# Kernel tuning notes

Measured on AMD Instinct MI355X. Metric: run time of the kernel, lower is better.

Reference implementation:

```python
import jax, jax.numpy as jnp
import numpy as np
from functools import partial

B, C, H, W = 256, 3, 128, 128

def _conv(x, w, b, pad):
    y = jax.lax.conv_general_dilated(x, w, (1, 1), [(pad, pad), (pad, pad)],
                                     dimension_numbers=('NCHW', 'OIHW', 'NCHW'))
    return y + b[None, :, None, None]

def _maxpool2(x):
    return jax.lax.reduce_window(x, -jnp.inf, jax.lax.max, (1, 1, 2, 2), (1, 1, 2, 2), 'VALID')

def _linear(x, w, b):
    return x @ w.T + b

def _handcrafted(images):
    # uint8 quantization: floor(x*255); inputs in [0,1) so no wraparound
    img8 = jnp.floor(images * 255.0)                      # [B,3,H,W]
    brightness = img8.mean(axis=(-2, -1))                 # [B,3]
    contrast = img8.std(axis=(-2, -1))                    # [B,3] (ddof=0, numpy default)
    # cv2.Sobel ksize=3, BORDER_REFLECT_101 == jnp.pad 'reflect'; cv2 does correlation
    kx = jnp.array([[-1., 0., 1.], [-2., 0., 2.], [-1., 0., 1.]], dtype=img8.dtype)
    ky = kx.T
    k = jnp.stack([kx, ky])[:, None]                      # [2,1,3,3]
    p = jnp.pad(img8, ((0, 0), (0, 0), (1, 1), (1, 1)), mode='reflect')
    s = jax.lax.conv_general_dilated(p.reshape(B * 3, 1, H + 2, W + 2), k, (1, 1),
                                     'VALID', dimension_numbers=('NCHW', 'OIHW', 'NCHW'))
    edge = jnp.sqrt(s[:, 0] ** 2 + s[:, 1] ** 2).mean(axis=(-2, -1)).reshape(B, 3)
    return jnp.concatenate([edge, brightness, contrast], axis=1)  # [B,9]

def setup_inputs() -> dict:
    key = jax.random.key(0)
    ks = jax.random.split(key, 20)
    g = lambda i, shape, fan: (jax.random.normal(ks[i], shape, jnp.float32) * (1.0 / np.sqrt(fan)))
    return {
        'images': jax.random.uniform(ks[0], (B, C, H, W), jnp.float32),
        'W1': g(1, (32, 3, 3, 3), 27), 'b1': jnp.zeros((32,), jnp.float32),
        'W2': g(2, (64, 32, 3, 3), 288), 'b2': jnp.zeros((64,), jnp.float32),
        'Wa': g(3, (1, 64, 7, 7), 64 * 49), 'ba': jnp.zeros((1,), jnp.float32),
        'Wfc': g(4, (50, 64 * 32 * 32), 64 * 32 * 32), 'bfc': jnp.zeros((50,), jnp.float32),
        'Wh1': g(5, (32, 9), 9), 'bh1': jnp.zeros((32,), jnp.float32),
        'Wh2': g(6, (64, 32), 32), 'bh2': jnp.zeros((64,), jnp.float32),
        'Wh3': g(7, (50, 64), 64), 'bh3': jnp.zeros((50,), jnp.float32),
        'Wf': g(8, (64, 100), 100), 'bf': jnp.zeros((64,), jnp.float32),
        'Wc': g(9, (1, 64), 64), 'bc': jnp.zeros((1,), jnp.float32),
    }

def reference(images, W1, b1, W2, b2, Wa, ba, Wfc, bfc,
              Wh1, bh1, Wh2, bh2, Wh3, bh3, Wf, bf, Wc, bc):
    # CNN branch
    x = jax.nn.relu(_conv(images, W1, b1, 1))
    x = _maxpool2(x)
    x = jax.nn.relu(_conv(x, W2, b2, 1))
    x = _maxpool2(x)                                      # [B,64,32,32]
    attn = jax.nn.sigmoid(_conv(x, Wa, ba, 3))            # spatial attention
    x = x * attn
    cnn_feat = jax.nn.relu(_linear(x.reshape(B, -1), Wfc, bfc))  # [B,50]
    # handcrafted branch
    f = _handcrafted(images)                              # [B,9]
    h = jax.nn.relu(_linear(f, Wh1, bh1))
    h = jax.nn.relu(_linear(h, Wh2, bh2))
    h = jax.nn.relu(_linear(h, Wh3, bh3))                 # [B,50]
    fused = jax.nn.relu(_linear(jnp.concatenate([cnn_feat, h], axis=1), Wf, bf))
    logits = _linear(fused, Wc, bc)
    return jax.nn.sigmoid(logits)
```

## Files before the change

### kernel.cpp

```cpp
#include <hip/hip_runtime.h>
#include <stdint.h>

typedef __bf16 bf16x8 __attribute__((ext_vector_type(8)));
typedef float f32x4 __attribute__((ext_vector_type(4)));

__device__ inline float bf2f(uint16_t u) {
    uint32_t x = ((uint32_t)u) << 16;
    float f;
    __builtin_memcpy(&f, &x, 4);
    return f;
}
__device__ inline uint16_t f2bf(float f) {
    uint32_t x;
    __builtin_memcpy(&x, &f, 4);
    uint32_t r = (x + 0x7FFFu + ((x >> 16) & 1u)) >> 16;
    return (uint16_t)r;
}

__global__ __launch_bounds__(256) void k_prep_small(const float* __restrict__ W2,
                                                    const float* __restrict__ W1,
                                                    const float* __restrict__ Wa,
                                                    uint16_t* __restrict__ wA,
                                                    uint16_t* __restrict__ wA1c,
                                                    uint16_t* __restrict__ waP) {
    int bid = blockIdx.x;
    int tid = threadIdx.x;
    if (bid < 72) {
        int j = bid * 256 + tid;
        if (j >= 18432) return;
        int t = j >> 11, rem = j & 2047, oc = rem >> 5, ic = rem & 31;
        int dy = t / 3, dx = t - dy * 3;
        wA[j] = f2bf(W2[(oc * 32 + ic) * 9 + dy * 3 + dx]);
    } else if (bid < 84) {
        int j = (bid - 72) * 256 + tid;
        if (j >= 3072) return;
        int dy = j >> 10, rem = j & 1023, oc = rem >> 5, k = rem & 31;
        int dx = k >> 2, ic = k & 3;
        uint16_t v = 0;
        if (dx < 3 && ic < 3) v = f2bf(W1[((oc * 3 + ic) * 3 + dy) * 3 + dx]);
        wA1c[j] = v;
    } else {
        int j = (bid - 84) * 256 + tid;
        if (j >= 4096) return;
        int chunk = j >> 10, ks = (j >> 9) & 1, tl = (j >> 5) & 15, ch = j & 31;
        int t = chunk * 16 + tl;
        int cg = ks * 32 + ch;
        waP[j] = (t < 49) ? f2bf(Wa[cg * 49 + t]) : (uint16_t)0;
    }
}

__global__ __launch_bounds__(256) void k_prep_wfc(const float* __restrict__ Wfc,
                                                  uint16_t* __restrict__ wfcb) {
    __shared__ uint16_t sT[64][132];
    int o = blockIdx.x;
    int px0 = blockIdx.y * 128;
    int tid = threadIdx.x;
#pragma unroll
    for (int p = 0; p < 8; ++p) {
        int idx = p * 256 + tid;
        int ch = idx >> 5, c4 = idx & 31;
        float4 v = *(const float4*)&Wfc[(size_t)o * 65536 + ch * 1024 + px0 + c4 * 4];
        ushort4 u;
        u.x = f2bf(v.x);
        u.y = f2bf(v.y);
        u.z = f2bf(v.z);
        u.w = f2bf(v.w);
        *(ushort4*)&sT[ch][c4 * 4] = u;
    }
    __syncthreads();
#pragma unroll
    for (int p = 0; p < 8; ++p) {
        int idx = p * 256 + tid;
        int pxl = idx >> 4, c = idx & 15;
        ushort4 u;
        u.x = sT[4 * c + 0][pxl];
        u.y = sT[4 * c + 1][pxl];
        u.z = sT[4 * c + 2][pxl];
        u.w = sT[4 * c + 3][pxl];
        *(ushort4*)&wfcb[(size_t)o * 65536 + (size_t)(px0 + pxl) * 64 + c * 4] = u;
    }
}

__global__ __launch_bounds__(256) void k_handcrafted(const float* __restrict__ img,
                                                     float* __restrict__ f) {
    __shared__ float p[128 * 129];
    int c = blockIdx.x, b = blockIdx.y;
    const float* src = img + (((size_t)(b * 3 + c)) << 14);
    int tid = threadIdx.x;
    float sum = 0.f, sumsq = 0.f;
    for (int it = 0; it < 64; ++it) {
        int idx = tid + (it << 8);
        int r = idx >> 7, cc = idx & 127;
        float v = floorf(src[idx] * 255.0f);
        p[r * 129 + cc] = v;
        sum += v;
        sumsq += v * v;
    }
    __syncthreads();
    {
        int r = tid >> 1;
        int c0 = (tid & 1) * 64;
        int rm = (r == 0) ? 1 : (r - 1), rp = (r == 127) ? 126 : (r + 1);
        const float* Pm = &p[rm * 129];
        const float* P0 = &p[r * 129];
        const float* Pp = &p[rp * 129];
        float am, a0, ap, bm, b0, bp, cm, c0v, cp;
        if (c0 == 0) {
            a0 = Pm[0]; ap = Pm[1]; am = ap;
            b0 = P0[0]; bp = P0[1]; bm = bp;
            c0v = Pp[0]; cp = Pp[1]; cm = cp;
        } else {
            am = Pm[63]; a0 = Pm[64]; ap = Pm[65];
            bm = P0[63]; b0 = P0[64]; bp = P0[65];
            cm = Pp[63]; c0v = Pp[64]; cp = Pp[65];
        }
        float esum = 0.f;
        for (int i = 0; i < 64; ++i) {
            float gx = (ap - am) + 2.f * (bp - bm) + (cp - cm);
            float gy = (cm + 2.f * c0v + cp) - (am + 2.f * a0 + ap);
            esum += sqrtf(gx * gx + gy * gy);
            if (i < 63) {
                int nc = c0 + i + 2;
                am = a0; a0 = ap;
                bm = b0; b0 = bp;
                cm = c0v; c0v = cp;
                if (nc <= 127) {
                    ap = Pm[nc];
                    bp = P0[nc];
                    cp = Pp[nc];
                } else {
                    ap = am;
                    bp = bm;
                    cp = cm;
                }
            }
        }
        for (int off = 32; off; off >>= 1) {
            sum += __shfl_down(sum, off);
            sumsq += __shfl_down(sumsq, off);
            esum += __shfl_down(esum, off);
        }
        __syncthreads();
        int w = tid >> 6;
        if ((tid & 63) == 0) {
            p[w * 3 + 0] = sum;
            p[w * 3 + 1] = sumsq;
            p[w * 3 + 2] = esum;
        }
        __syncthreads();
        if (tid == 0) {
            float S = 0.f, Q = 0.f, E = 0.f;
            for (int i = 0; i < 4; ++i) {
                S += p[i * 3 + 0];
                Q += p[i * 3 + 1];
                E += p[i * 3 + 2];
            }
            const float inv = 1.0f / 16384.0f;
            float mean = S * inv;
            float var = Q * inv - mean * mean;
            f[b * 16 + c] = E * inv;
            f[b * 16 + 3 + c] = mean;
            f[b * 16 + 6 + c] = sqrtf(fmaxf(var, 0.f));
        }
    }
}

__global__ __launch_bounds__(256) void k_conv1_mfma(const float* __restrict__ img,
                                                    const uint16_t* __restrict__ wA1c,
                                                    const float* __restrict__ b1,
                                                    uint16_t* __restrict__ pooled1) {
    __shared__ uint16_t s_nhwc[18 * 34 * 4 + 32];
    __shared__ uint16_t s_out[8 * 16 * 32];
    const int tile = blockIdx.x;
    const int b = blockIdx.y;
    const int ty = tile >> 2, tx = tile & 3;
    const int Y0 = ty * 16, X0 = tx * 32;
    const int tid = threadIdx.x;

    for (int j = tid; j < 612; j += 256) {
        int r = j / 34, sc = j - r * 34;
        int gy = Y0 - 1 + r, gx = X0 - 1 + sc;
        uint16_t d[4] = {0, 0, 0, 0};
        if ((unsigned)gy < 128u && (unsigned)gx < 128u) {
            size_t base = (((size_t)b * 3) << 14) + (gy << 7) + gx;
#pragma unroll
            for (int ic = 0; ic < 3; ++ic) d[ic] = f2bf(img[base + ((size_t)ic << 14)]);
        }
        *(uint2*)&s_nhwc[j * 4] = *(uint2*)d;
    }

    const int wv = tid >> 6, lane = tid & 63;
    const int rowl = lane & 15, kg = lane >> 4;

    bf16x8 afr[3][2];
#pragma unroll
    for (int dy = 0; dy < 3; ++dy)
#pragma unroll
        for (int g = 0; g < 2; ++g)
            afr[dy][g] = *(const bf16x8*)(wA1c + dy * 1024 + (g * 16 + rowl) * 32 + kg * 8);
    float bias[2][4];
#pragma unroll
    for (int g = 0; g < 2; ++g)
#pragma unroll
        for (int r = 0; r < 4; ++r)
            bias[g][r] = b1[g * 16 + kg * 4 + r];

    __syncthreads();

#pragma unroll
    for (int pr = 0; pr < 2; ++pr) {
#pragma unroll
        for (int seg = 0; seg < 2; ++seg) {
            const int y0 = wv * 4 + pr * 2;
            const int xl = seg * 16 + rowl;
            bf16x8 bw[4];
#pragma unroll
            for (int rr = 0; rr < 4; ++rr) {
                const uint16_t* rp = &s_nhwc[((y0 + rr) * 34 + xl + kg * 2) * 4];
                uint2 lo = *(const uint2*)rp;
                uint2 hi = *(const uint2*)(rp + 4);
                union { uint2 u[2]; bf16x8 v; } u;
                u.u[0] = lo;
                u.u[1] = hi;
                bw[rr] = u.v;
            }
            f32x4 acc0[2], acc1[2];
#pragma unroll
            for (int g = 0; g < 2; ++g)
#pragma unroll
                for (int r = 0; r < 4; ++r) {
                    acc0[g][r] = bias[g][r];
                    acc1[g][r] = bias[g][r];
                }
#pragma unroll
            for (int dy = 0; dy < 3; ++dy)
#pragma unroll
                for (int g = 0; g < 2; ++g) {
                    acc0[g] = __builtin_amdgcn_mfma_f32_16x16x32_bf16(afr[dy][g], bw[dy], acc0[g], 0, 0, 0);
                    acc1[g] = __builtin_amdgcn_mfma_f32_16x16x32_bf16(afr[dy][g], bw[dy + 1], acc1[g], 0, 0, 0);
                }
#pragma unroll
            for (int g = 0; g < 2; ++g)
#pragma unroll
                for (int r = 0; r < 4; ++r) {
                    float m = fmaxf(acc0[g][r], acc1[g][r]);
                    m = fmaxf(m, 0.f);
                    float o = fmaxf(m, __shfl_xor(m, 1));
                    if (!(lane & 1)) {
                        int prow = wv * 2 + pr;
                        int pcol = seg * 8 + (rowl >> 1);
                        int oc = g * 16 + kg * 4 + r;
                        s_out[(prow * 16 + pcol) * 32 + oc] = f2bf(o);
                    }
                }
        }
    }
    __syncthreads();
    for (int u = tid; u < 512; u += 256) {
        int px = u >> 2, c = u & 3;
        int prow = px >> 4, pcol = px & 15;
        uint4 v = *(const uint4*)&s_out[px * 32 + c * 8];
        ((uint4*)pooled1)[((((size_t)b << 12) + (ty * 8 + prow) * 64 + tx * 16 + pcol) << 2) + c] = v;
    }
}

__global__ __launch_bounds__(256) void k_conv2_mfma(const uint16_t* __restrict__ pooled1,
                                                    const uint16_t* __restrict__ wA,
                                                    const float* __restrict__ b2v,
                                                    uint16_t* __restrict__ pooled2n) {
    __shared__ uint16_t s_in[10 * 34 * 32];
    __shared__ uint16_t s_out[64 * 64];
    const int bx = blockIdx.x;
    const int b = blockIdx.y;
    const int tx = bx >> 3, ty = bx & 7;
    const int X0 = tx * 32, Y0 = ty * 8;
    const int tid = threadIdx.x;

    for (int j = tid; j < 1360; j += 256) {
        int r = j / 136;
        int rem = j - r * 136;
        int px = rem >> 2, c4 = rem & 3;
        int gy = Y0 - 1 + r, gx = X0 - 1 + px;
        uint4 v = make_uint4(0, 0, 0, 0);
        if ((unsigned)gy < 64u && (unsigned)gx < 64u)
            v = ((const uint4*)pooled1)[((((size_t)b << 12) + gy * 64 + gx) << 2) + c4];
        *(uint4*)&s_in[(r * 34 + px) * 32 + c4 * 8] = v;
    }

    const int wv = tid >> 6, lane = tid & 63;
    const int ocq = wv & 1, xth = wv >> 1;
    const int rowl = lane & 15, kg = lane >> 4;

    bf16x8 afr[9][2];
#pragma unroll
    for (int t = 0; t < 9; ++t)
#pragma unroll
        for (int g = 0; g < 2; ++g)
            afr[t][g] = *(const bf16x8*)(wA + t * 2048 + (ocq * 32 + g * 16 + rowl) * 32 + kg * 8);
    float bias[2][4];
#pragma unroll
    for (int g = 0; g < 2; ++g)
#pragma unroll
        for (int r = 0; r < 4; ++r)
            bias[g][r] = b2v[ocq * 32 + g * 16 + kg * 4 + r];

    __syncthreads();

    for (int yp = 0; yp < 4; ++yp) {
        f32x4 acc[2][2];
#pragma unroll
        for (int p = 0; p < 2; ++p)
#pragma unroll
            for (int g = 0; g < 2; ++g)
#pragma unroll
                for (int r = 0; r < 4; ++r) acc[p][g][r] = bias[g][r];

        bf16x8 bfr[4][3];
#pragma unroll
        for (int rr = 0; rr < 4; ++rr)
#pragma unroll
            for (int dx = 0; dx < 3; ++dx) {
                int pix = (2 * yp + rr) * 34 + xth * 16 + rowl + dx;
                bfr[rr][dx] = *(const bf16x8*)(s_in + pix * 32 + kg * 8);
            }
#pragma unroll
        for (int dy = 0; dy < 3; ++dy)
#pragma unroll
            for (int dx = 0; dx < 3; ++dx) {
                int t = dy * 3 + dx;
#pragma unroll
                for (int g = 0; g < 2; ++g) {
                    acc[0][g] = __builtin_amdgcn_mfma_f32_16x16x32_bf16(afr[t][g], bfr[dy][dx], acc[0][g], 0, 0, 0);
                    acc[1][g] = __builtin_amdgcn_mfma_f32_16x16x32_bf16(afr[t][g], bfr[dy + 1][dx], acc[1][g], 0, 0, 0);
                }
            }
#pragma unroll
        for (int g = 0; g < 2; ++g)
#pragma unroll
            for (int r = 0; r < 4; ++r) {
                float m = fmaxf(acc[0][g][r], acc[1][g][r]);
                m = fmaxf(m, 0.f);
                float o = fmaxf(m, __shfl_xor(m, 1));
                if (!(lane & 1)) {
                    int oc = ocq * 32 + g * 16 + kg * 4 + r;
                    int pxl = xth * 8 + (rowl >> 1);
                    int pl = yp * 16 + pxl;
                    s_out[pl * 64 + (oc ^ ((pxl & 7) << 3))] = f2bf(o);
                }
            }
    }
    __syncthreads();
    const int PY0 = ty * 4, PX0 = tx * 16;
    for (int u = tid; u < 512; u += 256) {
        int pl = u >> 3, c = u & 7;
        int py = pl >> 4, pxl = pl & 15;
        uint4 v = *(const uint4*)&s_out[pl * 64 + ((c ^ (pxl & 7)) << 3)];
        *(uint4*)&pooled2n[((((size_t)b << 10) + (PY0 + py) * 32 + PX0 + pxl) << 6) + c * 8] = v;
    }
}

__global__ __launch_bounds__(256) void k_attn_gemm(const uint16_t* __restrict__ pooled2n,
                                                   const uint16_t* __restrict__ waP,
                                                   const float* __restrict__ ba,
                                                   float* __restrict__ attn) {
    __shared__ uint16_t P[448 * 70];
    const int qt = blockIdx.x;
    const int b = blockIdx.y;
    const int tid = threadIdx.x;
    const int R0 = qt * 8;
    const int wv = tid >> 6, lane = tid & 63;
    const int rowl = lane & 15, kg = lane >> 4;

    bf16x8 afr[4][2];
#pragma unroll
    for (int c = 0; c < 4; ++c)
#pragma unroll
        for (int ks = 0; ks < 2; ++ks)
            afr[c][ks] = *(const bf16x8*)(waP + ((c * 2 + ks) * 16 + rowl) * 32 + kg * 8);

    for (int nt = wv; nt < 28; nt += 4) {
        int hpx = nt * 16 + rowl;
        int hrow = hpx >> 5, hcol = hpx & 31;
        int gy = R0 - 3 + hrow;
        bf16x8 bf0, bf1;
        if ((unsigned)gy < 32u) {
            const uint16_t* src = pooled2n + ((((size_t)b << 10) + (gy << 5) + hcol) << 6);
            bf0 = *(const bf16x8*)(src + kg * 8);
            bf1 = *(const bf16x8*)(src + 32 + kg * 8);
        } else {
            union { uint4 u; bf16x8 v; } z;
            z.u = make_uint4(0, 0, 0, 0);
            bf0 = z.v;
            bf1 = z.v;
        }
        f32x4 acc[4];
#pragma unroll
        for (int c = 0; c < 4; ++c)
#pragma unroll
            for (int r = 0; r < 4; ++r) acc[c][r] = 0.f;
#pragma unroll
        for (int c = 0; c < 4; ++c) {
            acc[c] = __builtin_amdgcn_mfma_f32_16x16x32_bf16(afr[c][0], bf0, acc[c], 0, 0, 0);
            acc[c] = __builtin_amdgcn_mfma_f32_16x16x32_bf16(afr[c][1], bf1, acc[c], 0, 0, 0);
        }
#pragma unroll
        for (int c = 0; c < 4; ++c) {
            uint32_t lo = (uint32_t)f2bf(acc[c][0]) | ((uint32_t)f2bf(acc[c][1]) << 16);
            uint32_t hi = (uint32_t)f2bf(acc[c][2]) | ((uint32_t)f2bf(acc[c][3]) << 16);
            uint16_t* dst = &P[hpx * 70 + c * 16 + kg * 4];
            *(uint32_t*)dst = lo;
            *(uint32_t*)(dst + 2) = hi;
        }
    }
    __syncthreads();

    const int pyl = tid >> 5, px = tid & 31;
    float v = ba[0];
#pragma unroll
    for (int dy = 0; dy < 7; ++dy) {
        int hl = pyl + dy;
#pragma unroll
        for (int dx = 0; dx < 7; ++dx) {
            int qx = px + dx - 3;
            if ((unsigned)qx < 32u) v += bf2f(P[(hl * 32 + qx) * 70 + dy * 7 + dx]);
        }
    }
    attn[((size_t)b << 10) + qt * 256 + tid] = 1.f / (1.f + __expf(-v));
}

__global__ __launch_bounds__(256) void k_fc_mfma(const uint16_t* __restrict__ pooled2n,
                                                 const float* __restrict__ attn,
                                                 const uint16_t* __restrict__ wfcb,
                                                 float* __restrict__ partial) {
    __shared__ uint16_t xh[128 * 128];
    const int wg = blockIdx.x;
    const int it = wg >> 6;
    const int kc = wg & 63;
    const int b0 = it * 16;
    const int K0 = kc * 1024;
    const int tid = threadIdx.x;

    for (int j = tid; j < 2048; j += 256) {
        int im = j >> 7, k8 = j & 127;
        int bimg = b0 + im;
        int gk = K0 + k8 * 8;
        int px = gk >> 6, ch0 = gk & 63;
        uint4 pv = *(const uint4*)&pooled2n[((((size_t)bimg << 10) + px) << 6) + ch0];
        float a = attn[((size_t)bimg << 10) + px];
        uint16_t s[8];
        *(uint4*)s = pv;
        uint16_t d[8];
#pragma unroll
        for (int i = 0; i < 8; ++i) d[i] = f2bf(bf2f(s[i]) * a);
        *(uint4*)&xh[k8 * 128 + im * 8] = *(uint4*)d;
    }

    const int wv = tid >> 6, lane = tid & 63;
    const int rowl = lane & 15, kg = lane >> 4;
    const uint16_t* wbase = wfcb + (size_t)(wv * 16 + rowl) * 65536 + K0 + kg * 8;

    __syncthreads();

    f32x4 acc = {0.f, 0.f, 0.f, 0.f};
#pragma unroll 4
    for (int kk = 0; kk < 32; ++kk) {
        bf16x8 af = *(const bf16x8*)(wbase + kk * 32);
        bf16x8 bf = *(const bf16x8*)&xh[(kk * 4 + kg) * 128 + rowl * 8];
        acc = __builtin_amdgcn_mfma_f32_16x16x32_bf16(af, bf, acc, 0, 0, 0);
    }
    float* pp = &partial[(((size_t)kc * 256 + (b0 + rowl)) << 6) + wv * 16 + kg * 4];
    *(f32x4*)pp = acc;
}

__global__ __launch_bounds__(64) void k_head(const float* __restrict__ fbuf,
                                             const float* __restrict__ partial,
                                             const float* __restrict__ Wh1, const float* __restrict__ bh1,
                                             const float* __restrict__ Wh2, const float* __restrict__ bh2,
                                             const float* __restrict__ Wh3, const float* __restrict__ bh3,
                                             const float* __restrict__ bfc,
                                             const float* __restrict__ Wf, const float* __restrict__ bf_,
                                             const float* __restrict__ Wc, const float* __restrict__ bc,
                                             float* __restrict__ out) {
    __shared__ float fl[9];
    __shared__ float h1[32];
    __shared__ float h2[64];
    __shared__ float cat[100];
    int b = blockIdx.x;
    int l = threadIdx.x;
    if (l < 9) fl[l] = fbuf[b * 16 + l];
    __syncthreads();
    if (l < 32) {
        float a = bh1[l];
        for (int i = 0; i < 9; ++i) a += fl[i] * Wh1[l * 9 + i];
        h1[l] = fmaxf(a, 0.f);
    }
    __syncthreads();
    {
        float a = bh2[l];
        for (int i = 0; i < 32; ++i) a += h1[i] * Wh2[l * 32 + i];
        h2[l] = fmaxf(a, 0.f);
    }
    __syncthreads();
    if (l < 50) {
        float a = bh3[l];
        for (int i = 0; i < 64; ++i) a += h2[i] * Wh3[l * 64 + i];
        cat[50 + l] = fmaxf(a, 0.f);
        float s = bfc[l];
        for (int kc2 = 0; kc2 < 64; ++kc2) s += partial[(((size_t)kc2 * 256 + b) << 6) + l];
        cat[l] = fmaxf(s, 0.f);
    }
    __syncthreads();
    float a = bf_[l];
    for (int i = 0; i < 100; ++i) a += cat[i] * Wf[l * 100 + i];
    a = fmaxf(a, 0.f);
    float v = a * Wc[l];
    for (int off = 32; off; off >>= 1) v += __shfl_down(v, off);
    if (l == 0) out[b] = 1.f / (1.f + __expf(-(v + bc[0])));
}

extern "C" void kernel_launch(void* const* d_in, const int* in_sizes, int n_in,
                              void* d_out, int out_size, void* d_ws, size_t ws_size,
                              hipStream_t stream) {
    const float* images = (const float*)d_in[0];
    const float* W1 = (const float*)d_in[1];
    const float* b1 = (const float*)d_in[2];
    const float* W2 = (const float*)d_in[3];
    const float* b2 = (const float*)d_in[4];
    const float* Wa = (const float*)d_in[5];
    const float* ba = (const float*)d_in[6];
    const float* Wfc = (const float*)d_in[7];
    const float* bfc = (const float*)d_in[8];
    const float* Wh1 = (const float*)d_in[9];
    const float* bh1 = (const float*)d_in[10];
    const float* Wh2 = (const float*)d_in[11];
    const float* bh2 = (const float*)d_in[12];
    const float* Wh3 = (const float*)d_in[13];
    const float* bh3 = (const float*)d_in[14];
    const float* Wf = (const float*)d_in[15];
    const float* bf_ = (const float*)d_in[16];
    const float* Wc = (const float*)d_in[17];
    const float* bc = (const float*)d_in[18];

    const size_t NEEDED = 102828032;
    if (ws_size < NEEDED) return;

    char* ws = (char*)d_ws;
    uint16_t* pooled1 = (uint16_t*)ws;
    uint16_t* pooled2n = (uint16_t*)(ws + 67108864);
    float* attn = (float*)(ws + 100663296);
    float* fbuf = (float*)(ws + 101711872);
    uint16_t* wA = (uint16_t*)(ws + 102776832);
    uint16_t* wA1c = (uint16_t*)(ws + 102813696);
    uint16_t* waP = (uint16_t*)(ws + 102819840);
    uint16_t* wfcb = (uint16_t*)ws;
    float* partial = (float*)(ws + 16777216);
    float* out = (float*)d_out;

    hipLaunchKernelGGL(k_prep_small, dim3(100), dim3(256), 0, stream, W2, W1, Wa, wA, wA1c, waP);
    hipLaunchKernelGGL(k_handcrafted, dim3(3, 256), dim3(256), 0, stream, images, fbuf);
    hipLaunchKernelGGL(k_conv1_mfma, dim3(32, 256), dim3(256), 0, stream, images, wA1c, b1, pooled1);
    hipLaunchKernelGGL(k_conv2_mfma, dim3(16, 256), dim3(256), 0, stream, pooled1, wA, b2, pooled2n);
    hipLaunchKernelGGL(k_prep_wfc, dim3(50, 8), dim3(256), 0, stream, Wfc, wfcb);
    hipLaunchKernelGGL(k_attn_gemm, dim3(4, 256), dim3(256), 0, stream, pooled2n, waP, ba, attn);
    hipLaunchKernelGGL(k_fc_mfma, dim3(1024), dim3(256), 0, stream, pooled2n, attn, wfcb, partial);
    hipLaunchKernelGGL(k_head, dim3(256), dim3(64), 0, stream, fbuf, partial,
                       Wh1, bh1, Wh2, bh2, Wh3, bh3, bfc, Wf, bf_, Wc, bc, out);
}
```

Baseline: 171.0 us.

## Merge independent kernels into combined launches and pack handcrafted image as uint8

Handcrafted features and conv1 now share one launch, split by block index; attention GEMM and Wfc bf16 transpose prep share another. This removes two kernel launches and lets independent work overlap on the GPU. The handcrafted branch now stores quantized pixels as uint8 in shared memory, loads with float4 and computes Sobel in integer arithmetic, which shrinks shared memory and raises occupancy. The merged kernels size LDS for the larger branch, which may lower occupancy of the smaller branch.

New measurement: 171.5 us. No clear change (+0.3%).

```diff
diff --git a/kernel.cpp b/kernel.cpp
--- a/kernel.cpp
+++ b/kernel.cpp
@@ -49,218 +49,205 @@
     }
 }
 
-__global__ __launch_bounds__(256) void k_prep_wfc(const float* __restrict__ Wfc,
-                                                  uint16_t* __restrict__ wfcb) {
-    __shared__ uint16_t sT[64][132];
-    int o = blockIdx.x;
-    int px0 = blockIdx.y * 128;
-    int tid = threadIdx.x;
-#pragma unroll
-    for (int p = 0; p < 8; ++p) {
-        int idx = p * 256 + tid;
-        int ch = idx >> 5, c4 = idx & 31;
-        float4 v = *(const float4*)&Wfc[(size_t)o * 65536 + ch * 1024 + px0 + c4 * 4];
-        ushort4 u;
-        u.x = f2bf(v.x);
-        u.y = f2bf(v.y);
-        u.z = f2bf(v.z);
-        u.w = f2bf(v.w);
-        *(ushort4*)&sT[ch][c4 * 4] = u;
-    }
-    __syncthreads();
-#pragma unroll
-    for (int p = 0; p < 8; ++p) {
-        int idx = p * 256 + tid;
-        int pxl = idx >> 4, c = idx & 15;
-        ushort4 u;
-        u.x = sT[4 * c + 0][pxl];
-        u.y = sT[4 * c + 1][pxl];
-        u.z = sT[4 * c + 2][pxl];
-        u.w = sT[4 * c + 3][pxl];
-        *(ushort4*)&wfcb[(size_t)o * 65536 + (size_t)(px0 + pxl) * 64 + c * 4] = u;
-    }
-}
-
-__global__ __launch_bounds__(256) void k_handcrafted(const float* __restrict__ img,
-                                                     float* __restrict__ f) {
-    __shared__ float p[128 * 129];
-    int c = blockIdx.x, b = blockIdx.y;
-    const float* src = img + (((size_t)(b * 3 + c)) << 14);
-    int tid = threadIdx.x;
-    float sum = 0.f, sumsq = 0.f;
-    for (int it = 0; it < 64; ++it) {
-        int idx = tid + (it << 8);
-        int r = idx >> 7, cc = idx & 127;
-        float v = floorf(src[idx] * 255.0f);
-        p[r * 129 + cc] = v;
-        sum += v;
-        sumsq += v * v;
-    }
-    __syncthreads();
+__global__ __launch_bounds__(256) void k_front(const float* __restrict__ img,
+                                               const uint16_t* __restrict__ wA1c,
+                                               const float* __restrict__ b1,
+                                               uint16_t* __restrict__ pooled1,
+                                               float* __restrict__ f) {
+    __shared__ __align__(16) uint8_t smem[16896];
+    const int bid = blockIdx.x;
+    const int tid = threadIdx.x;
+
+    if (bid < 768) {
+        int c = bid >> 8, b = bid & 255;
+        const float* src = img + (((size_t)(b * 3 + c)) << 14);
+        uint8_t* u8 = smem;
+        float sum = 0.f, sumsq = 0.f;
+        for (int it = 0; it < 16; ++it) {
+            int p4 = (it << 10) + (tid << 2);
+            float4 v = *(const float4*)&src[p4];
+            float f0 = floorf(v.x * 255.f), f1 = floorf(v.y * 255.f);
+            float f2 = floorf(v.z * 255.f), f3 = floorf(v.w * 255.f);
+            uint32_t pk = (uint32_t)(int)f0 | ((uint32_t)(int)f1 << 8) |
+                          ((uint32_t)(int)f2 << 16) | ((uint32_t)(int)f3 << 24);
+            int r = p4 >> 7, cc = p4 & 127;
+            *(uint32_t*)(u8 + r * 132 + cc) = pk;
+            sum += f0 + f1 + f2 + f3;
+            sumsq += f0 * f0 + f1 * f1 + f2 * f2 + f3 * f3;
+        }
+        __syncthreads();
+        {
+            int r = tid >> 1;
+            int c0 = (tid & 1) << 6;
+            int rm = (r == 0) ? 1 : r - 1, rp = (r == 127) ? 126 : r + 1;
+            const uint8_t* Rt = u8 + rm * 132;
+            const uint8_t* Rc = u8 + r * 132;
+            const uint8_t* Rb = u8 + rp * 132;
+            uint32_t wt = *(const uint32_t*)(Rt + c0);
+            uint32_t wm = *(const uint32_t*)(Rc + c0);
+            uint32_t wb = *(const uint32_t*)(Rb + c0);
+            int lt, lm, lb;
+            if (c0 == 0) {
+                lt = (wt >> 8) & 255; lm = (wm >> 8) & 255; lb = (wb >> 8) & 255;
+            } else {
+                lt = Rt[63]; lm = Rc[63]; lb = Rb[63];
+            }
+            float esum = 0.f;
+            for (int ch = 0; ch < 16; ++ch) {
+                int cb = c0 + (ch << 2);
+                bool hn = (cb + 4) < 128;
+                uint32_t nt = 0, nm = 0, nb = 0;
+                if (hn) {
+                    nt = *(const uint32_t*)(Rt + cb + 4);
+                    nm = *(const uint32_t*)(Rc + cb + 4);
+                    nb = *(const uint32_t*)(Rb + cb + 4);
+                }
+                int t[6], m[6], bo[6];
+                t[0] = lt; m[0] = lm; bo[0] = lb;
+#pragma unroll
+                for (int i = 0; i < 4; ++i) {
+                    t[i + 1] = (wt >> (8 * i)) & 255;
+                    m[i + 1] = (wm >> (8 * i)) & 255;
+                    bo[i + 1] = (wb >> (8 * i)) & 255;
+                }
+                t[5] = hn ? (int)(nt & 255) : (int)((wt >> 16) & 255);
+                m[5] = hn ? (int)(nm & 255) : (int)((wm >> 16) & 255);
+                bo[5] = hn ? (int)(nb & 255) : (int)((wb >> 16) & 255);
+#pragma unroll
+                for (int i = 0; i < 4; ++i) {
+                    int gx = (t[i + 2] - t[i]) + 2 * (m[i + 2] - m[i]) + (bo[i + 2] - bo[i]);
+                    int gy = (bo[i] + 2 * bo[i + 1] + bo[i + 2]) - (t[i] + 2 * t[i + 1] + t[i + 2]);
+                    esum += sqrtf((float)(gx * gx + gy * gy));
+                }
+                lt = t[4]; lm = m[4]; lb = bo[4];
+                wt = nt; wm = nm; wb = nb;
+            }
+            for (int off = 32; off; off >>= 1) {
+                sum += __shfl_down(sum, off);
+                sumsq += __shfl_down(sumsq, off);
+                esum += __shfl_down(esum, off);
+            }
+            __syncthreads();
+            float* scratch = (float*)smem;
+            int w = tid >> 6;
+            if ((tid & 63) == 0) {
+                scratch[w * 3 + 0] = sum;
+                scratch[w * 3 + 1] = sumsq;
+                scratch[w * 3 + 2] = esum;
+            }
+            __syncthreads();
+            if (tid == 0) {
+                float S = 0.f, Q = 0.f, E = 0.f;
+                for (int i = 0; i < 4; ++i) {
+                    S += scratch[i * 3 + 0];
+                    Q += scratch[i * 3 + 1];
+                    E += scratch[i * 3 + 2];
+                }
+                const float inv = 1.0f / 16384.0f;
+                float mean = S * inv;
+                float var = Q * inv - mean * mean;
+                f[b * 16 + c] = E * inv;
+                f[b * 16 + 3 + c] = mean;
+                f[b * 16 + 6 + c] = sqrtf(fmaxf(var, 0.f));
+            }
+        }
+        return;
+    }
+
     {
-        int r = tid >> 1;
-        int c0 = (tid & 1) * 64;
-        int rm = (r == 0) ? 1 : (r - 1), rp = (r == 127) ? 126 : (r + 1);
-        const float* Pm = &p[rm * 129];
-        const float* P0 = &p[r * 129];
-        const float* Pp = &p[rp * 129];
-        float am, a0, ap, bm, b0, bp, cm, c0v, cp;
-        if (c0 == 0) {
-            a0 = Pm[0]; ap = Pm[1]; am = ap;
-            b0 = P0[0]; bp = P0[1]; bm = bp;
-            c0v = Pp[0]; cp = Pp[1]; cm = cp;
-        } else {
-            am = Pm[63]; a0 = Pm[64]; ap = Pm[65];
-            bm = P0[63]; b0 = P0[64]; bp = P0[65];
-            cm = Pp[63]; c0v = Pp[64]; cp = Pp[65];
-        }
-        float esum = 0.f;
-        for (int i = 0; i < 64; ++i) {
-            float gx = (ap - am) + 2.f * (bp - bm) + (cp - cm);
-            float gy = (cm + 2.f * c0v + cp) - (am + 2.f * a0 + ap);
-            esum += sqrtf(gx * gx + gy * gy);
-            if (i < 63) {
-                int nc = c0 + i + 2;
-                am = a0; a0 = ap;
-                bm = b0; b0 = bp;
-                cm = c0v; c0v = cp;
-                if (nc <= 127) {
-                    ap = Pm[nc];
-                    bp = P0[nc];
-                    cp = Pp[nc];
-                } else {
-                    ap = am;
-                    bp = bm;
-                    cp = cm;
-                }
-            }
-        }
-        for (int off = 32; off; off >>= 1) {
-            sum += __shfl_down(sum, off);
-            sumsq += __shfl_down(sumsq, off);
-            esum += __shfl_down(esum, off);
-        }
+        uint16_t* s_out = (uint16_t*)smem;
+        uint16_t* s_nhwc = (uint16_t*)(smem + 8192);
+        const int j0 = bid - 768;
+        const int tile = j0 & 31;
+        const int b = j0 >> 5;
+        const int ty = tile >> 2, tx = tile & 3;
+        const int Y0 = ty * 16, X0 = tx * 32;
+
+        for (int j = tid; j < 612; j += 256) {
+            int r = j / 34, sc = j - r * 34;
+            int gy = Y0 - 1 + r, gx = X0 - 1 + sc;
+            uint16_t d[4] = {0, 0, 0, 0};
+            if ((unsigned)gy < 128u && (unsigned)gx < 128u) {
+                size_t base = (((size_t)b * 3) << 14) + (gy << 7) + gx;
+#pragma unroll
+                for (int ic = 0; ic < 3; ++ic) d[ic] = f2bf(img[base + ((size_t)ic << 14)]);
+            }
+            *(uint2*)&s_nhwc[j * 4] = *(uint2*)d;
+        }
+
+        const int wv = tid >> 6, lane = tid & 63;
+        const int rowl = lane & 15, kg = lane >> 4;
+
+        bf16x8 afr[3][2];
+#pragma unroll
+        for (int dy = 0; dy < 3; ++dy)
+#pragma unroll
+            for (int g = 0; g < 2; ++g)
+                afr[dy][g] = *(const bf16x8*)(wA1c + dy * 1024 + (g * 16 + rowl) * 32 + kg * 8);
+        float bias[2][4];
+#pragma unroll
+        for (int g = 0; g < 2; ++g)
+#pragma unroll
+            for (int r = 0; r < 4; ++r)
+                bias[g][r] = b1[g * 16 + kg * 4 + r];
+
         __syncthreads();
-        int w = tid >> 6;
-        if ((tid & 63) == 0) {
-            p[w * 3 + 0] = sum;
-            p[w * 3 + 1] = sumsq;
-            p[w * 3 + 2] = esum;
+
+#pragma unroll
+        for (int pr = 0; pr < 2; ++pr) {
+#pragma unroll
+            for (int seg = 0; seg < 2; ++seg) {
+                const int y0 = wv * 4 + pr * 2;
+                const int xl = seg * 16 + rowl;
+                bf16x8 bw[4];
+#pragma unroll
+                for (int rr = 0; rr < 4; ++rr) {
+                    const uint16_t* rp = &s_nhwc[((y0 + rr) * 34 + xl + kg * 2) * 4];
+                    uint2 lo = *(const uint2*)rp;
+                    uint2 hi = *(const uint2*)(rp + 4);
+                    union { uint2 u[2]; bf16x8 v; } u;
+                    u.u[0] = lo;
+                    u.u[1] = hi;
+                    bw[rr] = u.v;
+                }
+                f32x4 acc0[2], acc1[2];
+#pragma unroll
+                for (int g = 0; g < 2; ++g)
+#pragma unroll
+                    for (int r = 0; r < 4; ++r) {
+                        acc0[g][r] = bias[g][r];
+                        acc1[g][r] = bias[g][r];
+                    }
+#pragma unroll
+                for (int dy = 0; dy < 3; ++dy)
+#pragma unroll
+                    for (int g = 0; g < 2; ++g) {
+                        acc0[g] = __builtin_amdgcn_mfma_f32_16x16x32_bf16(afr[dy][g], bw[dy], acc0[g], 0, 0, 0);
+                        acc1[g] = __builtin_amdgcn_mfma_f32_16x16x32_bf16(afr[dy][g], bw[dy + 1], acc1[g], 0, 0, 0);
+                    }
+#pragma unroll
+                for (int g = 0; g < 2; ++g)
+#pragma unroll
+                    for (int r = 0; r < 4; ++r) {
+                        float m = fmaxf(acc0[g][r], acc1[g][r]);
+                        m = fmaxf(m, 0.f);
+                        float o = fmaxf(m, __shfl_xor(m, 1));
+                        if (!(lane & 1)) {
+                            int prow = wv * 2 + pr;
+                            int pcol = seg * 8 + (rowl >> 1);
+                            int oc = g * 16 + kg * 4 + r;
+                            s_out[(prow * 16 + pcol) * 32 + oc] = f2bf(o);
+                        }
+                    }
+            }
         }
         __syncthreads();
-        if (tid == 0) {
-            float S = 0.f, Q = 0.f, E = 0.f;
-            for (int i = 0; i < 4; ++i) {
-                S += p[i * 3 + 0];
-                Q += p[i * 3 + 1];
-                E += p[i * 3 + 2];
-            }
-            const float inv = 1.0f / 16384.0f;
-            float mean = S * inv;
-            float var = Q * inv - mean * mean;
-            f[b * 16 + c] = E * inv;
-            f[b * 16 + 3 + c] = mean;
-            f[b * 16 + 6 + c] = sqrtf(fmaxf(var, 0.f));
-        }
-    }
-}
-
-__global__ __launch_bounds__(256) void k_conv1_mfma(const float* __restrict__ img,
-                                                    const uint16_t* __restrict__ wA1c,
-                                                    const float* __restrict__ b1,
-                                                    uint16_t* __restrict__ pooled1) {
-    __shared__ uint16_t s_nhwc[18 * 34 * 4 + 32];
-    __shared__ uint16_t s_out[8 * 16 * 32];
-    const int tile = blockIdx.x;
-    const int b = blockIdx.y;
-    const int ty = tile >> 2, tx = tile & 3;
-    const int Y0 = ty * 16, X0 = tx * 32;
-    const int tid = threadIdx.x;
-
-    for (int j = tid; j < 612; j += 256) {
-        int r = j / 34, sc = j - r * 34;
-        int gy = Y0 - 1 + r, gx = X0 - 1 + sc;
-        uint16_t d[4] = {0, 0, 0, 0};
-        if ((unsigned)gy < 128u && (unsigned)gx < 128u) {
-            size_t base = (((size_t)b * 3) << 14) + (gy << 7) + gx;
-#pragma unroll
-            for (int ic = 0; ic < 3; ++ic) d[ic] = f2bf(img[base + ((size_t)ic << 14)]);
-        }
-        *(uint2*)&s_nhwc[j * 4] = *(uint2*)d;
-    }
-
-    const int wv = tid >> 6, lane = tid & 63;
-    const int rowl = lane & 15, kg = lane >> 4;
-
-    bf16x8 afr[3][2];
-#pragma unroll
-    for (int dy = 0; dy < 3; ++dy)
-#pragma unroll
-        for (int g = 0; g < 2; ++g)
-            afr[dy][g] = *(const bf16x8*)(wA1c + dy * 1024 + (g * 16 + rowl) * 32 + kg * 8);
-    float bias[2][4];
-#pragma unroll
-    for (int g = 0; g < 2; ++g)
-#pragma unroll
-        for (int r = 0; r < 4; ++r)
-            bias[g][r] = b1[g * 16 + kg * 4 + r];
-
-    __syncthreads();
-
-#pragma unroll
-    for (int pr = 0; pr < 2; ++pr) {
-#pragma unroll
-        for (int seg = 0; seg < 2; ++seg) {
-            const int y0 = wv * 4 + pr * 2;
-            const int xl = seg * 16 + rowl;
-            bf16x8 bw[4];
-#pragma unroll
-            for (int rr = 0; rr < 4; ++rr) {
-                const uint16_t* rp = &s_nhwc[((y0 + rr) * 34 + xl + kg * 2) * 4];
-                uint2 lo = *(const uint2*)rp;
-                uint2 hi = *(const uint2*)(rp + 4);
-                union { uint2 u[2]; bf16x8 v; } u;
-                u.u[0] = lo;
-                u.u[1] = hi;
-                bw[rr] = u.v;
-            }
-            f32x4 acc0[2], acc1[2];
-#pragma unroll
-            for (int g = 0; g < 2; ++g)
-#pragma unroll
-                for (int r = 0; r < 4; ++r) {
-                    acc0[g][r] = bias[g][r];
-                    acc1[g][r] = bias[g][r];
-                }
-#pragma unroll
-            for (int dy = 0; dy < 3; ++dy)
-#pragma unroll
-                for (int g = 0; g < 2; ++g) {
-                    acc0[g] = __builtin_amdgcn_mfma_f32_16x16x32_bf16(afr[dy][g], bw[dy], acc0[g], 0, 0, 0);
-                    acc1[g] = __builtin_amdgcn_mfma_f32_16x16x32_bf16(afr[dy][g], bw[dy + 1], acc1[g], 0, 0, 0);
-                }
-#pragma unroll
-            for (int g = 0; g < 2; ++g)
-#pragma unroll
-                for (int r = 0; r < 4; ++r) {
-                    float m = fmaxf(acc0[g][r], acc1[g][r]);
-                    m = fmaxf(m, 0.f);
-                    float o = fmaxf(m, __shfl_xor(m, 1));
-                    if (!(lane & 1)) {
-                        int prow = wv * 2 + pr;
-                        int pcol = seg * 8 + (rowl >> 1);
-                        int oc = g * 16 + kg * 4 + r;
-                        s_out[(prow * 16 + pcol) * 32 + oc] = f2bf(o);
-                    }
-                }
-        }
-    }
-    __syncthreads();
-    for (int u = tid; u < 512; u += 256) {
-        int px = u >> 2, c = u & 3;
-        int prow = px >> 4, pcol = px & 15;
-        uint4 v = *(const uint4*)&s_out[px * 32 + c * 8];
-        ((uint4*)pooled1)[((((size_t)b << 12) + (ty * 8 + prow) * 64 + tx * 16 + pcol) << 2) + c] = v;
+        for (int u = tid; u < 512; u += 256) {
+            int px = u >> 2, c = u & 3;
+            int prow = px >> 4, pcol = px & 15;
+            uint4 v = *(const uint4*)&s_out[px * 32 + c * 8];
+            ((uint4*)pooled1)[((((size_t)b << 12) + (ty * 8 + prow) * 64 + tx * 16 + pcol) << 2) + c] = v;
+        }
     }
 }
 
@@ -359,73 +346,112 @@
     }
 }
 
-__global__ __launch_bounds__(256) void k_attn_gemm(const uint16_t* __restrict__ pooled2n,
-                                                   const uint16_t* __restrict__ waP,
-                                                   const float* __restrict__ ba,
-                                                   float* __restrict__ attn) {
-    __shared__ uint16_t P[448 * 70];
-    const int qt = blockIdx.x;
-    const int b = blockIdx.y;
+__global__ __launch_bounds__(256) void k_mid(const uint16_t* __restrict__ pooled2n,
+                                             const uint16_t* __restrict__ waP,
+                                             const float* __restrict__ ba,
+                                             float* __restrict__ attn,
+                                             const float* __restrict__ Wfc,
+                                             uint16_t* __restrict__ wfcb) {
+    __shared__ __align__(16) uint8_t smem[62720];
+    const int bid = blockIdx.x;
     const int tid = threadIdx.x;
-    const int R0 = qt * 8;
-    const int wv = tid >> 6, lane = tid & 63;
-    const int rowl = lane & 15, kg = lane >> 4;
-
-    bf16x8 afr[4][2];
-#pragma unroll
-    for (int c = 0; c < 4; ++c)
-#pragma unroll
-        for (int ks = 0; ks < 2; ++ks)
-            afr[c][ks] = *(const bf16x8*)(waP + ((c * 2 + ks) * 16 + rowl) * 32 + kg * 8);
-
-    for (int nt = wv; nt < 28; nt += 4) {
-        int hpx = nt * 16 + rowl;
-        int hrow = hpx >> 5, hcol = hpx & 31;
-        int gy = R0 - 3 + hrow;
-        bf16x8 bf0, bf1;
-        if ((unsigned)gy < 32u) {
-            const uint16_t* src = pooled2n + ((((size_t)b << 10) + (gy << 5) + hcol) << 6);
-            bf0 = *(const bf16x8*)(src + kg * 8);
-            bf1 = *(const bf16x8*)(src + 32 + kg * 8);
-        } else {
-            union { uint4 u; bf16x8 v; } z;
-            z.u = make_uint4(0, 0, 0, 0);
-            bf0 = z.v;
-            bf1 = z.v;
-        }
-        f32x4 acc[4];
+
+    if (bid < 1024) {
+        uint16_t* P = (uint16_t*)smem;
+        const int qt = bid & 3;
+        const int b = bid >> 2;
+        const int R0 = qt * 8;
+        const int wv = tid >> 6, lane = tid & 63;
+        const int rowl = lane & 15, kg = lane >> 4;
+
+        bf16x8 afr[4][2];
 #pragma unroll
         for (int c = 0; c < 4; ++c)
 #pragma unroll
-            for (int r = 0; r < 4; ++r) acc[c][r] = 0.f;
-#pragma unroll
-        for (int c = 0; c < 4; ++c) {
-            acc[c] = __builtin_amdgcn_mfma_f32_16x16x32_bf16(afr[c][0], bf0, acc[c], 0, 0, 0);
-            acc[c] = __builtin_amdgcn_mfma_f32_16x16x32_bf16(afr[c][1], bf1, acc[c], 0, 0, 0);
-        }
-#pragma unroll
-        for (int c = 0; c < 4; ++c) {
-            uint32_t lo = (uint32_t)f2bf(acc[c][0]) | ((uint32_t)f2bf(acc[c][1]) << 16);
-            uint32_t hi = (uint32_t)f2bf(acc[c][2]) | ((uint32_t)f2bf(acc[c][3]) << 16);
-            uint16_t* dst = &P[hpx * 70 + c * 16 + kg * 4];
-            *(uint32_t*)dst = lo;
-            *(uint32_t*)(dst + 2) = hi;
-        }
-    }
-    __syncthreads();
-
-    const int pyl = tid >> 5, px = tid & 31;
-    float v = ba[0];
-#pragma unroll
-    for (int dy = 0; dy < 7; ++dy) {
-        int hl = pyl + dy;
-#pragma unroll
-        for (int dx = 0; dx < 7; ++dx) {
-            int qx = px + dx - 3;
-            if ((unsigned)qx < 32u) v += bf2f(P[(hl * 32 + qx) * 70 + dy * 7 + dx]);
-        }
-    }
-    attn[((size_t)b << 10) + qt * 256 + tid] = 1.f / (1.f + __expf(-v));
+            for (int ks = 0; ks < 2; ++ks)
+                afr[c][ks] = *(const bf16x8*)(waP + ((c * 2 + ks) * 16 + rowl) * 32 + kg * 8);
+
+        for (int nt = wv; nt < 28; nt += 4) {
+            int hpx = nt * 16 + rowl;
+            int hrow = hpx >> 5, hcol = hpx & 31;
+            int gy = R0 - 3 + hrow;
+            bf16x8 bf0, bf1;
+            if ((unsigned)gy < 32u) {
+                const uint16_t* src = pooled2n + ((((size_t)b << 10) + (gy << 5) + hcol) << 6);
+                bf0 = *(const bf16x8*)(src + kg * 8);
+                bf1 = *(const bf16x8*)(src + 32 + kg * 8);
+            } else {
+                union { uint4 u; bf16x8 v; } z;
+                z.u = make_uint4(0, 0, 0, 0);
+                bf0 = z.v;
+                bf1 = z.v;
+            }
+            f32x4 acc[4];
+#pragma unroll
+            for (int c = 0; c < 4; ++c)
+#pragma unroll
+                for (int r = 0; r < 4; ++r) acc[c][r] = 0.f;
+#pragma unroll
+            for (int c = 0; c < 4; ++c) {
+                acc[c] = __builtin_amdgcn_mfma_f32_16x16x32_bf16(afr[c][0], bf0, acc[c], 0, 0, 0);
+                acc[c] = __builtin_amdgcn_mfma_f32_16x16x32_bf16(afr[c][1], bf1, acc[c], 0, 0, 0);
+            }
+#pragma unroll
+            for (int c = 0; c < 4; ++c) {
+                uint32_t lo = (uint32_t)f2bf(acc[c][0]) | ((uint32_t)f2bf(acc[c][1]) << 16);
+                uint32_t hi = (uint32_t)f2bf(acc[c][2]) | ((uint32_t)f2bf(acc[c][3]) << 16);
+                uint16_t* dst = &P[hpx * 70 + c * 16 + kg * 4];
+                *(uint32_t*)dst = lo;
+                *(uint32_t*)(dst + 2) = hi;
+            }
+        }
+        __syncthreads();
+
+        const int pyl = tid >> 5, px = tid & 31;
+        float v = ba[0];
+#pragma unroll
+        for (int dy = 0; dy < 7; ++dy) {
+            int hl = pyl + dy;
+#pragma unroll
+            for (int dx = 0; dx < 7; ++dx) {
+                int qx = px + dx - 3;
+                if ((unsigned)qx < 32u) v += bf2f(P[(hl * 32 + qx) * 70 + dy * 7 + dx]);
+            }
+        }
+        attn[((size_t)b << 10) + qt * 256 + tid] = 1.f / (1.f + __expf(-v));
+        return;
+    }
+
+    {
+        uint16_t(*sT)[132] = (uint16_t(*)[132])smem;
+        int j0 = bid - 1024;
+        int o = j0 >> 3;
+        int px0 = (j0 & 7) * 128;
+#pragma unroll
+        for (int p = 0; p < 8; ++p) {
+            int idx = p * 256 + tid;
+            int ch = idx >> 5, c4 = idx & 31;
+            float4 v = *(const float4*)&Wfc[(size_t)o * 65536 + ch * 1024 + px0 + c4 * 4];
+            ushort4 u;
+            u.x = f2bf(v.x);
+            u.y = f2bf(v.y);
+            u.z = f2bf(v.z);
+            u.w = f2bf(v.w);
+            *(ushort4*)&sT[ch][c4 * 4] = u;
+        }
+        __syncthreads();
+#pragma unroll
+        for (int p = 0; p < 8; ++p) {
+            int idx = p * 256 + tid;
+            int pxl = idx >> 4, c = idx & 15;
+            ushort4 u;
+            u.x = sT[4 * c + 0][pxl];
+            u.y = sT[4 * c + 1][pxl];
+            u.z = sT[4 * c + 2][pxl];
+            u.w = sT[4 * c + 3][pxl];
+            *(ushort4*)&wfcb[(size_t)o * 65536 + (size_t)(px0 + pxl) * 64 + c * 4] = u;
+        }
+    }
 }
 
 __global__ __launch_bounds__(256) void k_fc_mfma(const uint16_t* __restrict__ pooled2n,
@@ -557,11 +583,9 @@
     float* out = (float*)d_out;
 
     hipLaunchKernelGGL(k_prep_small, dim3(100), dim3(256), 0, stream, W2, W1, Wa, wA, wA1c, waP);
-    hipLaunchKernelGGL(k_handcrafted, dim3(3, 256), dim3(256), 0, stream, images, fbuf);
-    hipLaunchKernelGGL(k_conv1_mfma, dim3(32, 256), dim3(256), 0, stream, images, wA1c, b1, pooled1);
+    hipLaunchKernelGGL(k_front, dim3(8960), dim3(256), 0, stream, images, wA1c, b1, pooled1, fbuf);
     hipLaunchKernelGGL(k_conv2_mfma, dim3(16, 256), dim3(256), 0, stream, pooled1, wA, b2, pooled2n);
-    hipLaunchKernelGGL(k_prep_wfc, dim3(50, 8), dim3(256), 0, stream, Wfc, wfcb);
-    hipLaunchKernelGGL(k_attn_gemm, dim3(4, 256), dim3(256), 0, stream, pooled2n, waP, ba, attn);
+    hipLaunchKernelGGL(k_mid, dim3(1424), dim3(256), 0, stream, pooled2n, waP, ba, attn, Wfc, wfcb);
     hipLaunchKernelGGL(k_fc_mfma, dim3(1024), dim3(256), 0, stream, pooled2n, attn, wfcb, partial);
     hipLaunchKernelGGL(k_head, dim3(256), dim3(64), 0, stream, fbuf, partial,
                        Wh1, bh1, Wh2, bh2, Wh3, bh3, bfc, Wf, bf_, Wc, bc, out);
```
